# Optimization experiments

Hardware: AMD Instinct MI355X
Metric: run time of the kernel (lower is better)

## Reference

```python
import jax, jax.numpy as jnp
import numpy as np
from jax import lax

D_MODEL = 128

def _pad_same(x, kh, kw):
    ph, pw = kh - 1, kw - 1
    return jnp.pad(x, ((0, 0), (0, 0), (ph // 2, ph - ph // 2), (pw // 2, pw - pw // 2)))

def _conv(x, w, b):
    y = lax.conv_general_dilated(x, w, (1, 1), 'VALID', dimension_numbers=('NCHW', 'OIHW', 'NCHW'))
    return y + b[None, :, None, None]

def _group_norm(x, g, b, groups, eps=1e-5):
    N, C, H, W = x.shape
    xr = x.reshape(N, groups, -1)
    m = xr.mean(axis=2, keepdims=True)
    v = xr.var(axis=2, keepdims=True)
    xn = ((xr - m) / jnp.sqrt(v + eps)).reshape(N, C, H, W)
    return xn * g[None, :, None, None] + b[None, :, None, None]

def _maxpool(x, kh, kw):
    return lax.reduce_window(x, -jnp.inf, lax.max, (1, 1, kh, kw), (1, 1, kh, kw), 'VALID')

def _l2norm(x, axis):
    # torch F.normalize(p=2): x / max(||x||, eps)
    return x / jnp.maximum(jnp.linalg.norm(x, axis=axis, keepdims=True), 1e-12)

def _pos_encoding(S, d):
    pos = jnp.arange(S, dtype=jnp.float32)[:, None]
    div = jnp.exp(jnp.arange(0, d, 2, dtype=jnp.float32) * (-float(np.log(10000.0)) / d))
    pe = jnp.zeros((S, d), dtype=jnp.float32)
    pe = pe.at[:, 0::2].set(jnp.sin(pos * div)).at[:, 1::2].set(jnp.cos(pos * div))
    return pe

def setup_inputs() -> dict:
    key = jax.random.key(0)
    ks = jax.random.split(key, 16)
    def w(k, shape, fan_in):
        return jax.random.normal(k, shape, dtype=jnp.float32) * (1.0 / np.sqrt(fan_in))
    return {
        'x': jax.random.normal(ks[0], (1, 1024, 72, 64), dtype=jnp.float32),
        'conv1_w': w(ks[1], (32, 1, 6, 4), 1 * 6 * 4),
        'conv1_b': jnp.zeros((32,), jnp.float32),
        'gn1_g': jnp.ones((32,), jnp.float32), 'gn1_b': jnp.zeros((32,), jnp.float32),
        'conv2_w': w(ks[2], (64, 32, 6, 4), 32 * 6 * 4),
        'conv2_b': jnp.zeros((64,), jnp.float32),
        'gn2_g': jnp.ones((64,), jnp.float32), 'gn2_b': jnp.zeros((64,), jnp.float32),
        'conv3_w': w(ks[3], (128, 64, 6, 4), 64 * 6 * 4),
        'conv3_b': jnp.zeros((128,), jnp.float32),
        'gn3_g': jnp.ones((128,), jnp.float32), 'gn3_b': jnp.zeros((128,), jnp.float32),
        'fc1_w': w(ks[4], (128, 1024), 1024),
        'fc1_b': jnp.zeros((128,), jnp.float32),
        'wq': w(ks[5], (128, 128), 128), 'bq': jnp.zeros((128,), jnp.float32),
        'wk': w(ks[6], (128, 128), 128), 'bk': jnp.zeros((128,), jnp.float32),
        'wv': w(ks[7], (128, 128), 128), 'bv': jnp.zeros((128,), jnp.float32),
    }

def reference(x, conv1_w, conv1_b, gn1_g, gn1_b, conv2_w, conv2_b, gn2_g, gn2_b,
              conv3_w, conv3_b, gn3_g, gn3_b, fc1_w, fc1_b, wq, bq, wk, bk, wv, bv):
    selu = jax.nn.selu
    # x: [1, S, 72, 64] -> transpose(0,1): [S, 1, 72, 64] (S frames, 1 channel)
    h = jnp.transpose(x, (1, 0, 2, 3))
    h = _maxpool(_group_norm(selu(_conv(_pad_same(h, 6, 4), conv1_w, conv1_b)), gn1_g, gn1_b, 32), 2, 4)
    h = _maxpool(_group_norm(selu(_conv(_pad_same(h, 6, 4), conv2_w, conv2_b)), gn2_g, gn2_b, 32), 3, 4)
    h = _maxpool(_group_norm(selu(_conv(_pad_same(h, 6, 4), conv3_w, conv3_b)), gn3_g, gn3_b, 32), 3, 2)
    e = h.reshape(h.shape[0], -1)                       # [S, 1024]
    e = _l2norm(selu(e @ fc1_w.T + fc1_b), axis=1)      # [S, 128]
    S = e.shape[0]
    q = selu(e @ wq.T + bq)
    k = selu(e @ wk.T + bk)
    v = selu(e @ wv.T + bv)
    k_pos = k + _pos_encoding(S, D_MODEL)               # PE added to K only
    attn = jax.nn.softmax((q @ k_pos.T) / jnp.sqrt(jnp.float32(D_MODEL)), axis=-1)  # [S, S]
    # torch F.normalize default dim=1 on [1,S,D] -> normalize over the sequence axis
    out = _l2norm(attn @ v, axis=0) + e
    ea = _l2norm(out, axis=0)                           # [S, 128]
    # pairwise L2 distances (self-similarity matrix), then 1 - d/max(d)
    sq = jnp.sum(ea * ea, axis=1)
    d2 = jnp.maximum(sq[:, None] + sq[None, :] - 2.0 * (ea @ ea.T), 0.0)
    d = jnp.sqrt(d2 + 1e-12)
    return 1.0 - d / jnp.max(d)
```

## Files before the change

kernel.cpp:

```cpp
#include <hip/hip_runtime.h>
#include <hip/hip_bf16.h>
#include <math.h>

#define SELU_SCALE 1.0507009873554805f
#define SELU_SA    1.7580993408473766f

typedef __attribute__((ext_vector_type(8))) short short8;
typedef __attribute__((ext_vector_type(4))) short short4v;
typedef __attribute__((ext_vector_type(4))) float f32x4;

__device__ __forceinline__ float selu_f(float x){
    return x > 0.f ? SELU_SCALE * x : fmaf(SELU_SA, __expf(x), -SELU_SA);
}

__device__ __forceinline__ unsigned short bfc(float v){
    __hip_bfloat16 h = __float2bfloat16(v);
    return __builtin_bit_cast(unsigned short, h);
}
__device__ __forceinline__ float f_bf(unsigned short u){
    unsigned int x = ((unsigned int)u) << 16;
    return __builtin_bit_cast(float, x);
}

__device__ __forceinline__ float warp_sum(float v){
    #pragma unroll
    for(int o=32;o>0;o>>=1) v += __shfl_down(v,o,64);
    return v;
}
__device__ __forceinline__ float warp_max(float v){
    #pragma unroll
    for(int o=32;o>0;o>>=1) v = fmaxf(v,__shfl_down(v,o,64));
    return v;
}

__device__ __forceinline__ void block_sum2(float &a, float &b, float* sred, int nw){
    int lane = threadIdx.x & 63, w = threadIdx.x >> 6;
    a = warp_sum(a); b = warp_sum(b);
    __syncthreads();
    if(lane==0){ sred[w]=a; sred[16+w]=b; }
    __syncthreads();
    if(w==0){
        float x = (lane<nw)? sred[lane] : 0.f;
        float y = (lane<nw)? sred[16+lane] : 0.f;
        x = warp_sum(x); y = warp_sum(y);
        if(lane==0){ sred[0]=x; sred[16]=y; }
    }
    __syncthreads();
    a = sred[0]; b = sred[16];
}

__device__ __forceinline__ float block_max_f(float v, float* sred, int nw){
    int lane = threadIdx.x & 63, w = threadIdx.x >> 6;
    v = warp_max(v);
    __syncthreads();
    if(lane==0) sred[w]=v;
    __syncthreads();
    if(w==0){
        float x = (lane<nw)? sred[lane] : -INFINITY;
        x = warp_max(x);
        if(lane==0) sred[0]=x;
    }
    __syncthreads();
    return sred[0];
}

__global__ void k_prep(const float* __restrict__ f1w, const float* __restrict__ wq,
                       const float* __restrict__ wk, const float* __restrict__ wv,
                       const float* __restrict__ w1, const float* __restrict__ w2,
                       const float* __restrict__ w3,
                       float* __restrict__ wt, float* __restrict__ wqt,
                       float* __restrict__ wkt, float* __restrict__ wvt,
                       short* __restrict__ w1bf, short* __restrict__ w2bf,
                       short* __restrict__ w3bf){
    int idx = blockIdx.x*256 + threadIdx.x;
    if(idx < 131072){ int r = idx >> 10, cc = idx & 1023; wt[cc*128 + r] = f1w[idx]; return; }
    idx -= 131072;
    if(idx < 16384){ int r = idx >> 7, cc = idx & 127; wqt[cc*128 + r] = wq[idx]; return; }
    idx -= 16384;
    if(idx < 16384){ int r = idx >> 7, cc = idx & 127; wkt[cc*128 + r] = wk[idx]; return; }
    idx -= 16384;
    if(idx < 16384){ int r = idx >> 7, cc = idx & 127; wvt[cc*128 + r] = wv[idx]; return; }
    idx -= 16384;
    if(idx < 49152){
        int t = idx >> 11, rem = idx & 2047;
        int oc = rem >> 5, ic = rem & 31;
        w2bf[idx] = (short)bfc(w2[oc*768 + ic*24 + t]);
        return;
    }
    idx -= 49152;
    if(idx < 196608){
        int t = idx >> 13, rem = idx & 8191;
        int oc = rem >> 6, ic = rem & 63;
        w3bf[idx] = (short)bfc(w3[oc*1536 + ic*24 + t]);
        return;
    }
    idx -= 196608;
    if(idx < 1024){
        int oc = idx >> 5, k = idx & 31;
        w1bf[idx] = (k < 24) ? (short)bfc(w1[oc*24 + k]) : (short)0;
    }
}

__global__ __launch_bounds__(768,1) void k_conv1m(
    const float* __restrict__ x, const short* __restrict__ w1bf,
    const float* __restrict__ bias, const float* __restrict__ g,
    const float* __restrict__ be, float* __restrict__ out)
{
    int s = blockIdx.x, tid = threadIdx.x;
    int l = tid & 63, wv = tid >> 6;
    int c = l & 15, qr = l >> 4;
    __shared__ char smem[117504];
    short* sdup = (short*)smem;
    char* pmaxb = smem + 40448;
    char* pminb = smem + 77312;
    float* sredf = (float*)(smem + 114176);
    __shared__ float scsh[64];

    const float* xs = x + (size_t)s*4608;
    for(int i = tid; i < 5056; i += 768){
        int yp = i >> 6, xx = i & 63;
        unsigned long long pk = 0ull;
        if(yp >= 2 && yp < 74){
            const float* row = xs + (yp-2)*64;
            #pragma unroll
            for(int t=0;t<4;t++){
                int cp = xx + t;
                float f = (cp>=1 && cp<65) ? row[cp-1] : 0.f;
                pk |= (unsigned long long)bfc(f) << (16*t);
            }
        }
        *(unsigned long long*)((char*)sdup + yp*512 + (xx&3)*128 + (xx>>2)*8) = pk;
    }
    short8 a0 = *(const short8*)(w1bf + c*32 + qr*8);
    short8 a1 = *(const short8*)(w1bf + (16+c)*32 + qr*8);
    float bias8[8];
    #pragma unroll
    for(int t=0;t<2;t++)
        #pragma unroll
        for(int r=0;r<4;r++) bias8[t*4+r] = bias[t*16 + qr*4 + r];
    float ssum8[8], ssq8[8];
    #pragma unroll
    for(int i=0;i<8;i++){ ssum8[i]=0.f; ssq8[i]=0.f; }
    __syncthreads();

    #pragma unroll 1
    for(int u=0; u<3; u++){
        int py = wv*3 + u;
        float pmx[8], pmn[8];
        #pragma unroll
        for(int i=0;i<8;i++){ pmx[i]=-INFINITY; pmn[i]=INFINITY; }
        #pragma unroll
        for(int off=0; off<4; off++){
            const char* bb = (const char*)sdup + off*128 + c*8;
            #pragma unroll
            for(int rr=0; rr<2; rr++){
                int y = py*2 + rr;
                short4v lo = *(const short4v*)(bb + (y+2*qr)*512);
                short4v hi = *(const short4v*)(bb + (y+2*qr+1)*512);
                short8 bfrag = __builtin_shufflevector(lo, hi, 0,1,2,3,4,5,6,7);
                f32x4 d0 = __builtin_amdgcn_mfma_f32_16x16x32_bf16(a0, bfrag, (f32x4){0.f,0.f,0.f,0.f}, 0,0,0);
                f32x4 d1 = __builtin_amdgcn_mfma_f32_16x16x32_bf16(a1, bfrag, (f32x4){0.f,0.f,0.f,0.f}, 0,0,0);
                #pragma unroll
                for(int r=0;r<4;r++){
                    float v0 = selu_f(d0[r] + bias8[r]);
                    float v1 = selu_f(d1[r] + bias8[4+r]);
                    ssum8[r]   += v0; ssq8[r]   = fmaf(v0,v0,ssq8[r]);
                    ssum8[4+r] += v1; ssq8[4+r] = fmaf(v1,v1,ssq8[4+r]);
                    pmx[r]   = fmaxf(pmx[r],   v0); pmn[r]   = fminf(pmn[r],   v0);
                    pmx[4+r] = fmaxf(pmx[4+r], v1); pmn[4+r] = fminf(pmn[4+r], v1);
                }
            }
        }
        int base = (py*16 + c)*64;
        #pragma unroll
        for(int t=0;t<2;t++){
            unsigned long long mpk=0ull, npk=0ull;
            #pragma unroll
            for(int r=0;r<4;r++){
                mpk |= (unsigned long long)bfc(pmx[t*4+r]) << (16*r);
                npk |= (unsigned long long)bfc(pmn[t*4+r]) << (16*r);
            }
            *(unsigned long long*)(pmaxb + base + t*32 + qr*8) = mpk;
            *(unsigned long long*)(pminb + base + t*32 + qr*8) = npk;
        }
    }
    #pragma unroll
    for(int off=1; off<16; off<<=1){
        #pragma unroll
        for(int i=0;i<8;i++){
            ssum8[i] += __shfl_xor(ssum8[i], off);
            ssq8[i]  += __shfl_xor(ssq8[i],  off);
        }
    }
    if(c == 0){
        #pragma unroll
        for(int i=0;i<8;i++){
            sredf[((wv*4 + qr)*8 + i)*2]     = ssum8[i];
            sredf[((wv*4 + qr)*8 + i)*2 + 1] = ssq8[i];
        }
    }
    __syncthreads();
    if(tid < 32){
        int oc = tid;
        int t = oc >> 4, rem = oc & 15, q = rem >> 2, r = rem & 3;
        int i = t*4 + r;
        float sum=0.f, sq=0.f;
        for(int w=0; w<12; w++){
            sum += sredf[((w*4+q)*8+i)*2];
            sq  += sredf[((w*4+q)*8+i)*2+1];
        }
        float mean = sum*(1.f/4608.f);
        float var  = sq*(1.f/4608.f) - mean*mean;
        float inv  = rsqrtf(var + 1e-5f);
        float sc = g[oc]*inv;
        scsh[oc*2]   = sc;
        scsh[oc*2+1] = be[oc] - mean*sc;
    }
    __syncthreads();
    float* ob = out + (size_t)s*18432;
    for(int i = tid; i < 18432; i += 768){
        int oc = i / 576, wpx = i - oc*576;
        float sc = scsh[oc*2], sh = scsh[oc*2+1];
        int boff = wpx*64 + oc*2;
        float vm = f_bf(*(unsigned short*)(pmaxb + boff));
        float vn = f_bf(*(unsigned short*)(pminb + boff));
        ob[i] = fmaf(sc, (sc >= 0.f) ? vm : vn, sh);
    }
}

__global__ __launch_bounds__(512,2) void k_conv2m(
    const float* __restrict__ in, const short* __restrict__ w2bf,
    const float* __restrict__ bias, const float* __restrict__ g,
    const float* __restrict__ be, float* __restrict__ out)
{
    int s = blockIdx.x, tid = threadIdx.x;
    int l = tid & 63, wv = tid >> 6;
    int ocp = wv >> 2, yq = wv & 3;
    int xc = l & 15, qr = l >> 4;
    __shared__ short sinb[26240];
    __shared__ float sred[2][4][2][4][2][2];
    int* zp = (int*)sinb;
    for(int i=tid;i<13120;i+=512) zp[i]=0;
    __syncthreads();
    const float* ibase = in + (size_t)s*18432;
    #pragma unroll
    for(int h=0;h<2;h++){
        int ic = (wv*2+h)*2;
        #pragma unroll
        for(int k=0;k<9;k++){
            int px = l + 64*k;
            float v0 = ibase[ic*576 + px];
            float v1 = ibase[(ic+1)*576 + px];
            int R = (px>>4)+2, C = (px&15)+1;
            int key = (C>>1)&3;
            int q0 = ic>>3;
            int byteoff = (R*20+C)*64 + (((q0^key)&3)<<4) + (ic&7)*2;
            *(unsigned int*)((char*)sinb + byteoff) =
                (unsigned int)bfc(v0) | ((unsigned int)bfc(v1)<<16);
        }
    }
    __syncthreads();
    f32x4 acc[2][9];
    #pragma unroll
    for(int o=0;o<2;o++)
        #pragma unroll
        for(int yt=0;yt<9;yt++) acc[o][yt] = (f32x4){0.f,0.f,0.f,0.f};
    const short8* wb = (const short8*)w2bf;
    int arow = ocp*32 + xc;
    short8 a0 = wb[arow*4 + qr];
    short8 a1 = wb[(arow+16)*4 + qr];
    char* sb = (char*)sinb;
    for(int tap=0; tap<24; tap++){
        short8 na0, na1;
        if(tap<23){
            na0 = wb[((tap+1)*64 + arow)*4 + qr];
            na1 = wb[((tap+1)*64 + arow + 16)*4 + qr];
        }
        int kh = tap>>2, kw = tap&3;
        int C = xc + kw;
        int cb = C*64 + (((qr ^ ((C>>1)&3))&3)<<4);
        int rb = (yq*9 + kh)*1280;
        #pragma unroll
        for(int yt=0;yt<9;yt++){
            short8 bf_ = *(const short8*)(sb + rb + yt*1280 + cb);
            acc[0][yt] = __builtin_amdgcn_mfma_f32_16x16x32_bf16(a0, bf_, acc[0][yt], 0,0,0);
            acc[1][yt] = __builtin_amdgcn_mfma_f32_16x16x32_bf16(a1, bf_, acc[1][yt], 0,0,0);
        }
        a0 = na0; a1 = na1;
    }
    #pragma unroll
    for(int o=0;o<2;o++){
        int ocb = (ocp*2+o)*16 + qr*4;
        float b0 = bias[ocb], b1 = bias[ocb+1], b2 = bias[ocb+2], b3 = bias[ocb+3];
        float s0=0,q0=0,s1=0,q1=0;
        #pragma unroll
        for(int yt=0;yt<9;yt++){
            float v0=selu_f(acc[o][yt][0]+b0), v1=selu_f(acc[o][yt][1]+b1);
            float v2=selu_f(acc[o][yt][2]+b2), v3=selu_f(acc[o][yt][3]+b3);
            acc[o][yt][0]=v0; acc[o][yt][1]=v1; acc[o][yt][2]=v2; acc[o][yt][3]=v3;
            s0+=v0+v1; q0+=v0*v0+v1*v1; s1+=v2+v3; q1+=v2*v2+v3*v3;
        }
        #pragma unroll
        for(int off=1;off<16;off<<=1){
            s0+=__shfl_xor(s0,off); q0+=__shfl_xor(q0,off);
            s1+=__shfl_xor(s1,off); q1+=__shfl_xor(q1,off);
        }
        if(xc==0){
            sred[ocp][yq][o][qr][0][0]=s0; sred[ocp][yq][o][qr][0][1]=q0;
            sred[ocp][yq][o][qr][1][0]=s1; sred[ocp][yq][o][qr][1][1]=q1;
        }
    }
    __syncthreads();
    float* ob = out + (size_t)s*64*48;
    #pragma unroll
    for(int o=0;o<2;o++){
        #pragma unroll
        for(int grp=0;grp<2;grp++){
            float ts=0, tq=0;
            #pragma unroll
            for(int y2=0;y2<4;y2++){ ts += sred[ocp][y2][o][qr][grp][0]; tq += sred[ocp][y2][o][qr][grp][1]; }
            float mean = ts*(1.f/1152.f);
            float var  = tq*(1.f/1152.f) - mean*mean;
            float inv  = rsqrtf(var + 1e-5f);
            int oc0 = (ocp*2+o)*16 + qr*4 + grp*2;
            float sc0 = g[oc0]*inv,   sh0 = be[oc0]   - mean*sc0;
            float sc1 = g[oc0+1]*inv, sh1 = be[oc0+1] - mean*sc1;
            #pragma unroll
            for(int yt=0;yt<9;yt++){
                acc[o][yt][grp*2]   = acc[o][yt][grp*2]*sc0 + sh0;
                acc[o][yt][grp*2+1] = acc[o][yt][grp*2+1]*sc1 + sh1;
            }
        }
        #pragma unroll
        for(int r=0;r<4;r++){
            #pragma unroll
            for(int py=0;py<3;py++){
                float m = fmaxf(fmaxf(acc[o][3*py][r],acc[o][3*py+1][r]),acc[o][3*py+2][r]);
                m = fmaxf(m, __shfl_xor(m,1));
                m = fmaxf(m, __shfl_xor(m,2));
                if((xc&3)==0){
                    int oc = (ocp*2+o)*16 + qr*4 + r;
                    ob[(size_t)oc*48 + (yq*3+py)*4 + (xc>>2)] = m;
                }
            }
        }
    }
}

__global__ __launch_bounds__(512,2) void k_conv3m(
    const float* __restrict__ in, const short* __restrict__ w3bf,
    const float* __restrict__ bias, const float* __restrict__ g,
    const float* __restrict__ be, float* __restrict__ e0)
{
    int sq = blockIdx.x, tid = threadIdx.x;
    int l = tid & 63, wv = tid >> 6;
    int ocp = wv >> 1, sL = wv & 1;
    int c = l & 15, qr = l >> 4;
    int yl = c >> 2, xl = c & 3;
    __shared__ char smem[49152];
    short* sinb = (short*)smem;
    int* zp = (int*)smem;
    for(int i=tid;i<8704;i+=512) zp[i]=0;
    __syncthreads();
    const float* ibase = in + (size_t)sq*6144;
    for(int j=0;j<6;j++){
        int idx = tid + 512*j;
        int px = idx % 48;
        int rest = idx / 48;
        int icp = rest & 31, ss = rest >> 5;
        int ic = icp*2;
        float v0 = ibase[ss*3072 + ic*48 + px];
        float v1 = ibase[ss*3072 + (ic+1)*48 + px];
        int R = (px>>2)+2, C = (px&3)+1;
        int pos = ss*136 + R*8 + C;
        int key = ((R&1)<<2) | (C&3);
        int q0 = ic>>3;
        int byteoff = pos*128 + (((q0^key)&7)<<4) + (ic&7)*2;
        *(unsigned int*)(smem + byteoff) = (unsigned int)bfc(v0) | ((unsigned int)bfc(v1)<<16);
    }
    __syncthreads();
    f32x4 acc[2][3];
    #pragma unroll
    for(int o=0;o<2;o++)
        #pragma unroll
        for(int yt=0;yt<3;yt++) acc[o][yt] = (f32x4){0.f,0.f,0.f,0.f};
    const short8* wb = (const short8*)w3bf;
    int arow = ocp*32 + c;
    char* sb = smem + sL*17408;
    short8 a0 = wb[arow*8 + qr];
    short8 a1 = wb[(arow+16)*8 + qr];
    for(int t2=0; t2<48; t2++){
        short8 na0, na1;
        if(t2<47){
            int nt = t2+1;
            na0 = wb[((nt>>1)*128 + arow)*8 + (nt&1)*4 + qr];
            na1 = wb[((nt>>1)*128 + arow + 16)*8 + (nt&1)*4 + qr];
        }
        int tap = t2>>1, ks = t2&1;
        int kh = tap>>2, kw = tap&3;
        int C = xl + kw;
        int q0 = ks*4 + qr;
        #pragma unroll
        for(int yt=0;yt<3;yt++){
            int R = yt*4 + yl + kh;
            int key = ((R&1)<<2) | (C&3);
            short8 bf_ = *(const short8*)(sb + (R*8+C)*128 + (((q0^key)&7)<<4));
            acc[0][yt] = __builtin_amdgcn_mfma_f32_16x16x32_bf16(a0, bf_, acc[0][yt], 0,0,0);
            acc[1][yt] = __builtin_amdgcn_mfma_f32_16x16x32_bf16(a1, bf_, acc[1][yt], 0,0,0);
        }
        a0 = na0; a1 = na1;
    }
    #pragma unroll
    for(int o=0;o<2;o++){
        int ocb = (ocp*2+o)*16 + qr*4;
        float b0 = bias[ocb], b1 = bias[ocb+1], b2 = bias[ocb+2], b3 = bias[ocb+3];
        float ssum=0.f, ssq=0.f;
        #pragma unroll
        for(int yt=0;yt<3;yt++){
            float v0=selu_f(acc[o][yt][0]+b0), v1=selu_f(acc[o][yt][1]+b1);
            float v2=selu_f(acc[o][yt][2]+b2), v3=selu_f(acc[o][yt][3]+b3);
            acc[o][yt][0]=v0; acc[o][yt][1]=v1; acc[o][yt][2]=v2; acc[o][yt][3]=v3;
            ssum += v0+v1+v2+v3; ssq += v0*v0+v1*v1+v2*v2+v3*v3;
        }
        #pragma unroll
        for(int off=1;off<16;off<<=1){ ssum+=__shfl_xor(ssum,off); ssq+=__shfl_xor(ssq,off); }
        float mean = ssum*(1.f/192.f);
        float var  = ssq*(1.f/192.f) - mean*mean;
        float inv  = rsqrtf(var + 1e-5f);
        #pragma unroll
        for(int r=0;r<4;r++){
            int oc = ocb + r;
            float sc = g[oc]*inv, sh = be[oc] - mean*sc;
            #pragma unroll
            for(int yt=0;yt<3;yt++) acc[o][yt][r] = acc[o][yt][r]*sc + sh;
        }
    }
    __syncthreads();
    float* scr = (float*)smem + wv*1536;
    #pragma unroll
    for(int o=0;o<2;o++)
        #pragma unroll
        for(int yt=0;yt<3;yt++)
            #pragma unroll
            for(int r=0;r<4;r++){
                int px = (yt*4+yl)*4 + xl;
                scr[o*768 + (qr*4+r)*48 + px] = acc[o][yt][r];
            }
    __syncthreads();
    float* sr = (float*)smem + wv*1536 + (l>>5)*768 + ((l>>1)&15)*48;
    int x2 = l&1;
    float* eo = e0 + (size_t)(sq*2+sL)*1024 + ((size_t)(ocp*2 + (l>>5))*16 + ((l>>1)&15))*8;
    #pragma unroll
    for(int py=0;py<4;py++){
        float m = sr[(py*3)*4 + x2*2];
        m = fmaxf(m, sr[(py*3)*4 + x2*2+1]);
        m = fmaxf(m, sr[(py*3+1)*4 + x2*2]);
        m = fmaxf(m, sr[(py*3+1)*4 + x2*2+1]);
        m = fmaxf(m, sr[(py*3+2)*4 + x2*2]);
        m = fmaxf(m, sr[(py*3+2)*4 + x2*2+1]);
        eo[py*2 + x2] = m;
    }
}

__global__ __launch_bounds__(256) void k_fc1(
    const float* __restrict__ e0, const float* __restrict__ wt,
    const float* __restrict__ bias, float* __restrict__ e)
{
    int s = blockIdx.x, tid = threadIdx.x;
    int j = tid & 127, half = tid >> 7;
    __shared__ float se[1024];
    __shared__ float sp[2][128];
    __shared__ float sred[2];
    for(int i=tid;i<1024;i+=256) se[i] = e0[(size_t)s*1024+i];
    __syncthreads();
    float acc = half ? 0.f : bias[j];
    const float* wp = wt + (size_t)half*512*128 + j;
    const float* sep = se + half*512;
    #pragma unroll 8
    for(int i=0;i<512;i++) acc += sep[i]*wp[(size_t)i*128];
    sp[half][j] = acc;
    __syncthreads();
    if(half==0){
        float v = selu_f(sp[0][j]+sp[1][j]);
        float a = v*v;
        #pragma unroll
        for(int o=1;o<64;o<<=1) a += __shfl_xor(a,o);
        if((j&63)==0) sred[j>>6]=a;
    }
    __syncthreads();
    if(half==0){
        float den = fmaxf(sqrtf(sred[0]+sred[1]), 1e-12f);
        float v = selu_f(sp[0][j]+sp[1][j]);
        e[(size_t)s*128+j] = v/den;
    }
}

__global__ __launch_bounds__(256) void k_qkv(
    const float* __restrict__ e,
    const float* __restrict__ wqt, const float* __restrict__ bq,
    const float* __restrict__ wkt, const float* __restrict__ bk,
    const float* __restrict__ wvt, const float* __restrict__ bv,
    float* __restrict__ q, float* __restrict__ kp, float* __restrict__ v)
{
    int s = blockIdx.x, tid = threadIdx.x;
    int j = tid & 127, half = tid >> 7;
    __shared__ float se[128];
    __shared__ float sp[3][2][128];
    if(tid < 128) se[tid] = e[(size_t)s*128+tid];
    __syncthreads();
    float aq = half?0.f:bq[j], ak = half?0.f:bk[j], av = half?0.f:bv[j];
    int i0 = half*64;
    #pragma unroll 8
    for(int i=i0;i<i0+64;i++){
        float f = se[i];
        aq += f*wqt[i*128+j];
        ak += f*wkt[i*128+j];
        av += f*wvt[i*128+j];
    }
    sp[0][half][j]=aq; sp[1][half][j]=ak; sp[2][half][j]=av;
    __syncthreads();
    if(half==0){
        float vq = selu_f(sp[0][0][j]+sp[0][1][j]);
        float vk = selu_f(sp[1][0][j]+sp[1][1][j]);
        float vv = selu_f(sp[2][0][j]+sp[2][1][j]);
        int i2 = j & ~1;
        float div = __expf(-(float)i2 * 0.07195578412155481f);
        float ang = (float)s * div;
        float pe = (j & 1) ? cosf(ang) : sinf(ang);
        q[(size_t)s*128+j]  = vq;
        kp[(size_t)s*128+j] = vk + pe;
        v[(size_t)s*128+j]  = vv;
    }
}

__global__ __launch_bounds__(256) void k_attn(
    const float* __restrict__ q, const float* __restrict__ kp, float* __restrict__ attn)
{
    int s = blockIdx.x, tid = threadIdx.x;
    __shared__ float sq_[128];
    __shared__ float sred[32];
    if(tid < 128) sq_[tid] = q[(size_t)s*128+tid];
    __syncthreads();
    float val[4];
    const float4* qr = (const float4*)sq_;
    #pragma unroll
    for(int k2=0;k2<4;k2++){
        int t = tid + k2*256;
        const float4* kr = (const float4*)(kp + (size_t)t*128);
        float acc=0.f;
        #pragma unroll 8
        for(int i=0;i<32;i++){
            float4 a=qr[i], b=kr[i];
            acc += a.x*b.x + a.y*b.y + a.z*b.z + a.w*b.w;
        }
        val[k2] = acc * 0.08838834764831845f;
    }
    float m = fmaxf(fmaxf(val[0],val[1]), fmaxf(val[2],val[3]));
    m = block_max_f(m,sred,4);
    float lsum=0.f, dummy=0.f;
    #pragma unroll
    for(int k2=0;k2<4;k2++){ val[k2]=__expf(val[k2]-m); lsum+=val[k2]; }
    block_sum2(lsum,dummy,sred,4);
    float invs = 1.f/lsum;
    #pragma unroll
    for(int k2=0;k2<4;k2++) attn[(size_t)s*1024 + tid + k2*256] = val[k2]*invs;
}

__global__ __launch_bounds__(256) void k_av(
    const float* __restrict__ attn, const float* __restrict__ v, float* __restrict__ av)
{
    int s = blockIdx.x, tid = threadIdx.x;
    int j = tid & 127, half = tid >> 7;
    __shared__ float sa[1024];
    __shared__ float spart[2][128];
    for(int i=tid;i<1024;i+=256) sa[i] = attn[(size_t)s*1024+i];
    __syncthreads();
    float acc=0.f;
    int t0 = half*512;
    for(int t=t0;t<t0+512;t++) acc += sa[t]*v[(size_t)t*128+j];
    spart[half][j] = acc;
    __syncthreads();
    if(half==0) av[(size_t)s*128+j] = spart[0][j] + spart[1][j];
}

__global__ __launch_bounds__(256) void k_colpipe(
    const float* __restrict__ av, const float* __restrict__ e, float* __restrict__ ea)
{
    int j = blockIdx.x, t = threadIdx.x;
    __shared__ float sred[4];
    float v[4];
    float ss = 0.f;
    #pragma unroll
    for(int k=0;k<4;k++){
        v[k] = av[(size_t)(t + 256*k)*128 + j];
        ss += v[k]*v[k];
    }
    #pragma unroll
    for(int off=1;off<64;off<<=1) ss += __shfl_xor(ss,off);
    int lane = t & 63, w = t >> 6;
    if(lane==0) sred[w]=ss;
    __syncthreads();
    float n1 = fmaxf(sqrtf(sred[0]+sred[1]+sred[2]+sred[3]), 1e-12f);
    __syncthreads();
    float ss2 = 0.f;
    #pragma unroll
    for(int k=0;k<4;k++){
        float o = v[k]/n1 + e[(size_t)(t + 256*k)*128 + j];
        v[k] = o;
        ss2 += o*o;
    }
    #pragma unroll
    for(int off=1;off<64;off<<=1) ss2 += __shfl_xor(ss2,off);
    if(lane==0) sred[w]=ss2;
    __syncthreads();
    float n2 = fmaxf(sqrtf(sred[0]+sred[1]+sred[2]+sred[3]), 1e-12f);
    #pragma unroll
    for(int k=0;k<4;k++) ea[(size_t)(t + 256*k)*128 + j] = v[k]/n2;
}

__global__ __launch_bounds__(128) void k_sq(const float* __restrict__ ea, float* __restrict__ sq){
    int s = blockIdx.x, j = threadIdx.x;
    __shared__ float sred[32];
    float v = ea[(size_t)s*128+j];
    float a=v*v, b=0.f;
    block_sum2(a,b,sred,2);
    if(j==0) sq[s]=a;
}

__global__ __launch_bounds__(256) void k_gram(
    const float* __restrict__ ea, const float* __restrict__ sq,
    float* __restrict__ d2, unsigned int* __restrict__ maxbits)
{
    int j0 = blockIdx.x*32, i0 = blockIdx.y*32, tid = threadIdx.x;
    __shared__ float sa[32*128];
    __shared__ float sb[32*128];
    __shared__ float sred[32];
    for(int idx=tid;idx<4096;idx+=256){
        sa[idx] = ea[(size_t)i0*128 + idx];
        sb[idx] = ea[(size_t)j0*128 + idx];
    }
    __syncthreads();
    float lm = 0.f;
    #pragma unroll
    for(int k2=0;k2<4;k2++){
        int p = tid + k2*256;
        int li = p>>5, lj = p&31;
        const float4* A = (const float4*)(sa + li*128);
        const float4* B = (const float4*)(sb + lj*128);
        float acc=0.f;
        #pragma unroll 8
        for(int i=0;i<32;i++){
            float4 a=A[i], b=B[i];
            acc += a.x*b.x + a.y*b.y + a.z*b.z + a.w*b.w;
        }
        float dd = fmaxf(sq[i0+li] + sq[j0+lj] - 2.f*acc, 0.f);
        d2[(size_t)(i0+li)*1024 + j0+lj] = dd;
        lm = fmaxf(lm, dd);
    }
    lm = block_max_f(lm,sred,4);
    if(tid==0) atomicMax(maxbits, __float_as_uint(lm));
}

__global__ __launch_bounds__(256) void k_final(
    const float* __restrict__ d2, const unsigned int* __restrict__ maxbits, float* __restrict__ out)
{
    int idx = blockIdx.x*256 + threadIdx.x;
    float md = sqrtf(__uint_as_float(*maxbits) + 1e-12f);
    out[idx] = 1.f - sqrtf(d2[idx] + 1e-12f)/md;
}

extern "C" void kernel_launch(void* const* d_in, const int* in_sizes, int n_in,
                              void* d_out, int out_size, void* d_ws, size_t ws_size,
                              hipStream_t stream)
{
    const float* x   = (const float*)d_in[0];
    const float* c1w = (const float*)d_in[1];  const float* c1b = (const float*)d_in[2];
    const float* g1g = (const float*)d_in[3];  const float* g1b = (const float*)d_in[4];
    const float* c2w = (const float*)d_in[5];  const float* c2b = (const float*)d_in[6];
    const float* g2g = (const float*)d_in[7];  const float* g2b = (const float*)d_in[8];
    const float* c3w = (const float*)d_in[9];  const float* c3b = (const float*)d_in[10];
    const float* g3g = (const float*)d_in[11]; const float* g3b = (const float*)d_in[12];
    const float* f1w = (const float*)d_in[13]; const float* f1b = (const float*)d_in[14];
    const float* wq  = (const float*)d_in[15]; const float* bq  = (const float*)d_in[16];
    const float* wk  = (const float*)d_in[17]; const float* bk  = (const float*)d_in[18];
    const float* wv  = (const float*)d_in[19]; const float* bv  = (const float*)d_in[20];

    float* W = (float*)d_ws;
    float* e0   = W;
    float* attn = W + 1048576;
    float* avb  = W + 2097152;
    float* eab  = W + 2228224;
    float* d2b  = W + 2359296;
    float* buf1 = W;
    float* buf2 = W + 18874368;
    float* wt   = W + 22020096;
    float* wqt  = W + 22151168;
    float* wkt  = W + 22167552;
    float* wvt  = W + 22183936;
    float* eb   = W + 22200320;
    float* qb   = W + 22331392;
    float* kpb  = W + 22462464;
    float* vb   = W + 22593536;
    float* sqb  = W + 22724608;
    unsigned int* maxb = (unsigned int*)(W + 22725632);
    short* w2bf = (short*)(W + 22725648);
    short* w3bf = (short*)(W + 22750224);
    short* w1bf = (short*)(W + 22848528);

    k_prep<<<1670,256,0,stream>>>(f1w, wq, wk, wv, c1w, c2w, c3w,
                                  wt, wqt, wkt, wvt, w1bf, w2bf, w3bf);

    k_conv1m<<<1024,768,0,stream>>>(x, w1bf, c1b, g1g, g1b, buf1);
    k_conv2m<<<1024,512,0,stream>>>(buf1, w2bf, c2b, g2g, g2b, buf2);
    k_conv3m<<<512,512,0,stream>>>(buf2, w3bf, c3b, g3g, g3b, e0);

    k_fc1<<<1024,256,0,stream>>>(e0, wt, f1b, eb);
    k_qkv<<<1024,256,0,stream>>>(eb, wqt,bq, wkt,bk, wvt,bv, qb,kpb,vb);
    k_attn<<<1024,256,0,stream>>>(qb, kpb, attn);
    k_av<<<1024,256,0,stream>>>(attn, vb, avb);

    hipMemsetAsync(maxb, 0, 4, stream);
    k_colpipe<<<128,256,0,stream>>>(avb, eb, eab);
    k_sq<<<1024,128,0,stream>>>(eab, sqb);
    k_gram<<<dim3(32,32),256,0,stream>>>(eab, sqb, d2b, maxb);
    k_final<<<4096,256,0,stream>>>(d2b, maxb, (float*)d_out);
}
```

Baseline: 422.4 us.

## Fuse fc1 with qkv and attention with AV; pad conv1 LDS rows

Merges the fc1 and QKV projection kernels into one, keeping the normalized embedding row in shared memory instead of reloading it from global. Merges the softmax attention kernel with the attention-times-V kernel, so the 1024x1024 attention matrix stays in shared memory and is never written to or read back from global memory. Also pads the conv1 shared-memory row strides (512 to 528 bytes, 64 to 72 bytes) to reduce LDS bank conflicts, which raises LDS use to about 128KB per block.

```diff
diff --git a/kernel.cpp b/kernel.cpp
--- a/kernel.cpp
+++ b/kernel.cpp
@@ -109,11 +109,11 @@
     int s = blockIdx.x, tid = threadIdx.x;
     int l = tid & 63, wv = tid >> 6;
     int c = l & 15, qr = l >> 4;
-    __shared__ char smem[117504];
+    __shared__ char smem[127728];
     short* sdup = (short*)smem;
-    char* pmaxb = smem + 40448;
-    char* pminb = smem + 77312;
-    float* sredf = (float*)(smem + 114176);
+    char* pmaxb = smem + 41712;
+    char* pminb = smem + 83184;
+    float* sredf = (float*)(smem + 124656);
     __shared__ float scsh[64];
 
     const float* xs = x + (size_t)s*4608;
@@ -129,7 +129,7 @@
                 pk |= (unsigned long long)bfc(f) << (16*t);
             }
         }
-        *(unsigned long long*)((char*)sdup + yp*512 + (xx&3)*128 + (xx>>2)*8) = pk;
+        *(unsigned long long*)((char*)sdup + yp*528 + (xx&3)*128 + (xx>>2)*8) = pk;
     }
     short8 a0 = *(const short8*)(w1bf + c*32 + qr*8);
     short8 a1 = *(const short8*)(w1bf + (16+c)*32 + qr*8);
@@ -155,8 +155,8 @@
             #pragma unroll
             for(int rr=0; rr<2; rr++){
                 int y = py*2 + rr;
-                short4v lo = *(const short4v*)(bb + (y+2*qr)*512);
-                short4v hi = *(const short4v*)(bb + (y+2*qr+1)*512);
+                short4v lo = *(const short4v*)(bb + (y+2*qr)*528);
+                short4v hi = *(const short4v*)(bb + (y+2*qr+1)*528);
                 short8 bfrag = __builtin_shufflevector(lo, hi, 0,1,2,3,4,5,6,7);
                 f32x4 d0 = __builtin_amdgcn_mfma_f32_16x16x32_bf16(a0, bfrag, (f32x4){0.f,0.f,0.f,0.f}, 0,0,0);
                 f32x4 d1 = __builtin_amdgcn_mfma_f32_16x16x32_bf16(a1, bfrag, (f32x4){0.f,0.f,0.f,0.f}, 0,0,0);
@@ -171,7 +171,7 @@
                 }
             }
         }
-        int base = (py*16 + c)*64;
+        int base = (py*16 + c)*72;
         #pragma unroll
         for(int t=0;t<2;t++){
             unsigned long long mpk=0ull, npk=0ull;
@@ -221,7 +221,7 @@
     for(int i = tid; i < 18432; i += 768){
         int oc = i / 576, wpx = i - oc*576;
         float sc = scsh[oc*2], sh = scsh[oc*2+1];
-        int boff = wpx*64 + oc*2;
+        int boff = wpx*72 + oc*2;
         float vm = f_bf(*(unsigned short*)(pmaxb + boff));
         float vn = f_bf(*(unsigned short*)(pminb + boff));
         ob[i] = fmaf(sc, (sc >= 0.f) ? vm : vn, sh);
@@ -462,15 +462,21 @@
     }
 }
 
-__global__ __launch_bounds__(256) void k_fc1(
+__global__ __launch_bounds__(256) void k_fcqkv(
     const float* __restrict__ e0, const float* __restrict__ wt,
-    const float* __restrict__ bias, float* __restrict__ e)
+    const float* __restrict__ bias, float* __restrict__ e,
+    const float* __restrict__ wqt, const float* __restrict__ bq,
+    const float* __restrict__ wkt, const float* __restrict__ bk,
+    const float* __restrict__ wvt, const float* __restrict__ bv,
+    float* __restrict__ q, float* __restrict__ kp, float* __restrict__ v)
 {
     int s = blockIdx.x, tid = threadIdx.x;
     int j = tid & 127, half = tid >> 7;
     __shared__ float se[1024];
     __shared__ float sp[2][128];
     __shared__ float sred[2];
+    __shared__ float se2[128];
+    __shared__ float sp3[3][2][128];
     for(int i=tid;i<1024;i+=256) se[i] = e0[(size_t)s*1024+i];
     __syncthreads();
     float acc = half ? 0.f : bias[j];
@@ -481,8 +487,8 @@
     sp[half][j] = acc;
     __syncthreads();
     if(half==0){
-        float v = selu_f(sp[0][j]+sp[1][j]);
-        float a = v*v;
+        float vv = selu_f(sp[0][j]+sp[1][j]);
+        float a = vv*vv;
         #pragma unroll
         for(int o=1;o<64;o<<=1) a += __shfl_xor(a,o);
         if((j&63)==0) sred[j>>6]=a;
@@ -490,39 +496,27 @@
     __syncthreads();
     if(half==0){
         float den = fmaxf(sqrtf(sred[0]+sred[1]), 1e-12f);
-        float v = selu_f(sp[0][j]+sp[1][j]);
-        e[(size_t)s*128+j] = v/den;
-    }
-}
-
-__global__ __launch_bounds__(256) void k_qkv(
-    const float* __restrict__ e,
-    const float* __restrict__ wqt, const float* __restrict__ bq,
-    const float* __restrict__ wkt, const float* __restrict__ bk,
-    const float* __restrict__ wvt, const float* __restrict__ bv,
-    float* __restrict__ q, float* __restrict__ kp, float* __restrict__ v)
-{
-    int s = blockIdx.x, tid = threadIdx.x;
-    int j = tid & 127, half = tid >> 7;
-    __shared__ float se[128];
-    __shared__ float sp[3][2][128];
-    if(tid < 128) se[tid] = e[(size_t)s*128+tid];
+        float vv = selu_f(sp[0][j]+sp[1][j]);
+        float ev = vv/den;
+        se2[j] = ev;
+        e[(size_t)s*128+j] = ev;
+    }
     __syncthreads();
     float aq = half?0.f:bq[j], ak = half?0.f:bk[j], av = half?0.f:bv[j];
     int i0 = half*64;
     #pragma unroll 8
     for(int i=i0;i<i0+64;i++){
-        float f = se[i];
+        float f = se2[i];
         aq += f*wqt[i*128+j];
         ak += f*wkt[i*128+j];
         av += f*wvt[i*128+j];
     }
-    sp[0][half][j]=aq; sp[1][half][j]=ak; sp[2][half][j]=av;
+    sp3[0][half][j]=aq; sp3[1][half][j]=ak; sp3[2][half][j]=av;
     __syncthreads();
     if(half==0){
-        float vq = selu_f(sp[0][0][j]+sp[0][1][j]);
-        float vk = selu_f(sp[1][0][j]+sp[1][1][j]);
-        float vv = selu_f(sp[2][0][j]+sp[2][1][j]);
+        float vq = selu_f(sp3[0][0][j]+sp3[0][1][j]);
+        float vk = selu_f(sp3[1][0][j]+sp3[1][1][j]);
+        float vv = selu_f(sp3[2][0][j]+sp3[2][1][j]);
         int i2 = j & ~1;
         float div = __expf(-(float)i2 * 0.07195578412155481f);
         float ang = (float)s * div;
@@ -533,12 +527,15 @@
     }
 }
 
-__global__ __launch_bounds__(256) void k_attn(
-    const float* __restrict__ q, const float* __restrict__ kp, float* __restrict__ attn)
+__global__ __launch_bounds__(256) void k_attnav(
+    const float* __restrict__ q, const float* __restrict__ kp,
+    const float* __restrict__ v, float* __restrict__ av)
 {
     int s = blockIdx.x, tid = threadIdx.x;
     __shared__ float sq_[128];
-    __shared__ float sred[32];
+    __shared__ float sredm[32];
+    __shared__ float spb[1024];
+    __shared__ float spart[2][128];
     if(tid < 128) sq_[tid] = q[(size_t)s*128+tid];
     __syncthreads();
     float val[4];
@@ -556,28 +553,19 @@
         val[k2] = acc * 0.08838834764831845f;
     }
     float m = fmaxf(fmaxf(val[0],val[1]), fmaxf(val[2],val[3]));
-    m = block_max_f(m,sred,4);
+    m = block_max_f(m,sredm,4);
     float lsum=0.f, dummy=0.f;
     #pragma unroll
     for(int k2=0;k2<4;k2++){ val[k2]=__expf(val[k2]-m); lsum+=val[k2]; }
-    block_sum2(lsum,dummy,sred,4);
+    block_sum2(lsum,dummy,sredm,4);
     float invs = 1.f/lsum;
     #pragma unroll
-    for(int k2=0;k2<4;k2++) attn[(size_t)s*1024 + tid + k2*256] = val[k2]*invs;
-}
-
-__global__ __launch_bounds__(256) void k_av(
-    const float* __restrict__ attn, const float* __restrict__ v, float* __restrict__ av)
-{
-    int s = blockIdx.x, tid = threadIdx.x;
+    for(int k2=0;k2<4;k2++) spb[tid + k2*256] = val[k2]*invs;
+    __syncthreads();
     int j = tid & 127, half = tid >> 7;
-    __shared__ float sa[1024];
-    __shared__ float spart[2][128];
-    for(int i=tid;i<1024;i+=256) sa[i] = attn[(size_t)s*1024+i];
-    __syncthreads();
     float acc=0.f;
     int t0 = half*512;
-    for(int t=t0;t<t0+512;t++) acc += sa[t]*v[(size_t)t*128+j];
+    for(int t=t0;t<t0+512;t++) acc += spb[t]*v[(size_t)t*128+j];
     spart[half][j] = acc;
     __syncthreads();
     if(half==0) av[(size_t)s*128+j] = spart[0][j] + spart[1][j];
@@ -687,7 +675,6 @@
 
     float* W = (float*)d_ws;
     float* e0   = W;
-    float* attn = W + 1048576;
     float* avb  = W + 2097152;
     float* eab  = W + 2228224;
     float* d2b  = W + 2359296;
@@ -714,10 +701,8 @@
     k_conv2m<<<1024,512,0,stream>>>(buf1, w2bf, c2b, g2g, g2b, buf2);
     k_conv3m<<<512,512,0,stream>>>(buf2, w3bf, c3b, g3g, g3b, e0);
 
-    k_fc1<<<1024,256,0,stream>>>(e0, wt, f1b, eb);
-    k_qkv<<<1024,256,0,stream>>>(eb, wqt,bq, wkt,bk, wvt,bv, qb,kpb,vb);
-    k_attn<<<1024,256,0,stream>>>(qb, kpb, attn);
-    k_av<<<1024,256,0,stream>>>(attn, vb, avb);
+    k_fcqkv<<<1024,256,0,stream>>>(e0, wt, f1b, eb, wqt,bq, wkt,bk, wvt,bv, qb,kpb,vb);
+    k_attnav<<<1024,256,0,stream>>>(qb, kpb, vb, avb);
 
     hipMemsetAsync(maxb, 0, 4, stream);
     k_colpipe<<<128,256,0,stream>>>(avb, eb, eab);
```

Result: faster. 387.9 us (-8.2%).
